# Kernel tuning notes

Hardware: AMD Instinct MI355X
Metric: run time of the kernel (lower is better)

## Reference

```python
import jax, jax.numpy as jnp
import numpy as np

TAU = 2.0  # self.temperature
EPS_GUMBEL = 1e-10
EPS_PPL = 1e-7


def setup_inputs() -> dict:
    key = jax.random.key(0)
    k1, k2, k3, k4, k5 = jax.random.split(key, 5)
    B, H = 65536, 512          # batch, conv_dim[-1]
    G, V, E = 2, 320, 256      # groups, codevectors per group, codevector_dim
    hidden_states = jax.random.normal(k1, (B, 1, H), dtype=jnp.float32)
    uniform_noise = jax.random.uniform(k2, (B, G, V), dtype=jnp.float32)
    embeddings = jax.random.uniform(k3, (G, V, E), dtype=jnp.float32, minval=-1.0, maxval=1.0)
    W_proj = jax.random.normal(k4, (G * V, H), dtype=jnp.float32) / np.sqrt(H)
    b_proj = jax.random.normal(k5, (G * V,), dtype=jnp.float32) * 0.01
    return {"hidden_states": hidden_states, "uniform_noise": uniform_noise,
            "embeddings": embeddings, "W_proj": W_proj, "b_proj": b_proj}


def reference(hidden_states, uniform_noise, embeddings, W_proj, b_proj):
    B = hidden_states.shape[0]
    G, V, E = embeddings.shape
    # weight_proj: (B, 1, H) -> (B, G*V) -> (B, G, V)
    x = hidden_states[:, 0, :]
    logits = (x @ W_proj.T + b_proj).reshape(B, G, V)
    # gumbel_softmax(tau=2, hard=True): straight-through hard one-hot
    g = -jnp.log(-jnp.log(uniform_noise + EPS_GUMBEL) + EPS_GUMBEL)
    y_soft = jax.nn.softmax((logits + g) / TAU, axis=-1)
    idx = jnp.argmax(y_soft, axis=-1)                              # (B, G)
    y_hard = jax.nn.one_hot(idx, V, dtype=y_soft.dtype)            # (B, G, V)
    gumbel_dist = y_hard - jax.lax.stop_gradient(y_soft) + y_soft  # ST estimator
    # perplexity over batch-marginal probabilities
    marginal = gumbel_dist.mean(axis=0)                            # (G, V)
    perplexity = jnp.exp(-jnp.sum(marginal * jnp.log(marginal + EPS_PPL), axis=-1)).sum()
    # select codevectors: (B, G, V) x (G, V, E) -> (B, G, E)
    selected = jnp.einsum('bgv,gve->bge', gumbel_dist, embeddings)
    return selected, perplexity
```

## Files before the change

### kernel.cpp

```cpp
#include <hip/hip_runtime.h>
#include <math.h>

#define H 512
#define GV 640
#define E_DIM 256
#define BM 64
#define KSTEP 32
#define NKT (H / KSTEP)

typedef _Float16 half8 __attribute__((ext_vector_type(8)));
typedef float f32x4 __attribute__((ext_vector_type(4)));

#define WS_WH 4096
#define WS_WL (4096 + 655360)
#define WS_NEED (4096 + 2 * 655360)

__global__ void prep_w(const float* __restrict__ W, _Float16* __restrict__ wh,
                       _Float16* __restrict__ wl)
{
    int t = blockIdx.x * 256 + threadIdx.x;
    int kt = t / 2560;
    int rem = t % 2560;
    int g = rem / 640;
    int col = rem - g * 640;
    int k = kt * KSTEP + g * 8;
    const float* src = W + (size_t)col * H + k;
    float4 v0 = *(const float4*)src;
    float4 v1 = *(const float4*)(src + 4);
    float vv[8] = {v0.x, v0.y, v0.z, v0.w, v1.x, v1.y, v1.z, v1.w};
    half8 hv, lv;
    #pragma unroll
    for (int i = 0; i < 8; ++i) {
        float ws_ = vv[i] * 1024.0f;
        _Float16 h = (_Float16)ws_;
        hv[i] = h;
        lv[i] = (_Float16)(ws_ - (float)h);
    }
    ((half8*)wh)[t] = hv;
    ((half8*)wl)[t] = lv;
}

__global__ __launch_bounds__(640) void gemm_argmax_mfma(
    const float* __restrict__ hid,
    const float* __restrict__ noise,
    const float* __restrict__ emb,
    const float* __restrict__ bias,
    const _Float16* __restrict__ wh,
    const _Float16* __restrict__ wl,
    float* __restrict__ out,
    int* __restrict__ cnt)
{
    __shared__ __align__(16) _Float16 Xh[BM][KSTEP];
    __shared__ __align__(16) _Float16 Xl[BM][KSTEP];
    __shared__ int sel_n[BM][2];

    float* red_val = (float*)&Xh[0][0];
    int*   red_idx = (int*)&Xl[0][0];

    const int tid = threadIdx.x;
    const int w = tid >> 6;
    const int l = tid & 63;
    const int q = l & 15, g = l >> 4;
    const int sig = (q >> 1) & 3;
    const int sl = (g ^ sig) * 8;
    const int brow = blockIdx.x * BM;

    f32x4 acc[4][4];
    #pragma unroll
    for (int mt = 0; mt < 4; ++mt)
        #pragma unroll
        for (int nt = 0; nt < 4; ++nt)
            acc[mt][nt] = (f32x4){0.f, 0.f, 0.f, 0.f};

    const half8* whv = (const half8*)wh;
    const half8* wlv = (const half8*)wl;

    for (int kt = 0; kt < NKT; ++kt) {
        __syncthreads();
        if (tid < 256) {
            int r = tid & 63, c = tid >> 6;
            const float* src = hid + (size_t)(brow + r) * H + kt * KSTEP + c * 8;
            float4 v0 = *(const float4*)src;
            float4 v1 = *(const float4*)(src + 4);
            float vv[8] = {v0.x, v0.y, v0.z, v0.w, v1.x, v1.y, v1.z, v1.w};
            half8 hv, lv;
            #pragma unroll
            for (int i = 0; i < 8; ++i) {
                float xs = vv[i] * 64.0f;
                _Float16 h = (_Float16)xs;
                hv[i] = h;
                lv[i] = (_Float16)(xs - (float)h);
            }
            int slot = c ^ ((r >> 1) & 3);
            *(half8*)&Xh[r][slot * 8] = hv;
            *(half8*)&Xl[r][slot * 8] = lv;
        }
        __syncthreads();

        half8 Ah[4], Al[4];
        #pragma unroll
        for (int mt = 0; mt < 4; ++mt) {
            int row = mt * 16 + q;
            Ah[mt] = *(const half8*)&Xh[row][sl];
            Al[mt] = *(const half8*)&Xl[row][sl];
        }

        const int gbase = (kt * 4 + g) * 640 + w * 64 + q;
        #pragma unroll
        for (int nt = 0; nt < 4; ++nt) {
            half8 Bh = whv[gbase + nt * 16];
            half8 Bl = wlv[gbase + nt * 16];
            #pragma unroll
            for (int mt = 0; mt < 4; ++mt) {
                acc[mt][nt] = __builtin_amdgcn_mfma_f32_16x16x32_f16(Ah[mt], Bh, acc[mt][nt], 0, 0, 0);
                acc[mt][nt] = __builtin_amdgcn_mfma_f32_16x16x32_f16(Ah[mt], Bl, acc[mt][nt], 0, 0, 0);
                acc[mt][nt] = __builtin_amdgcn_mfma_f32_16x16x32_f16(Al[mt], Bh, acc[mt][nt], 0, 0, 0);
            }
        }
    }

    __syncthreads();

    const float C1 = 1.52587890625e-05f;
    float bcol[4];
    #pragma unroll
    for (int nt = 0; nt < 4; ++nt) bcol[nt] = bias[w * 64 + nt * 16 + q];

    #pragma unroll
    for (int mt = 0; mt < 4; ++mt) {
        #pragma unroll
        for (int reg = 0; reg < 4; ++reg) {
            int r = mt * 16 + 4 * g + reg;
            float bv = -INFINITY;
            int bn = 0;
            #pragma unroll
            for (int nt = 0; nt < 4; ++nt) {
                int col = w * 64 + nt * 16 + q;
                float u = noise[(size_t)(brow + r) * GV + col];
                float gum = -logf(-logf(u + 1e-10f) + 1e-10f);
                float z = acc[mt][nt][reg] * C1 + bcol[nt] + gum;
                if (z > bv) { bv = z; bn = col; }
            }
            #pragma unroll
            for (int m = 1; m < 16; m <<= 1) {
                float ov = __shfl_xor(bv, m, 64);
                int on = __shfl_xor(bn, m, 64);
                if (ov > bv || (ov == bv && on < bn)) { bv = ov; bn = on; }
            }
            if (q == 0) { red_val[r * 10 + w] = bv; red_idx[r * 10 + w] = bn; }
        }
    }
    __syncthreads();

    if (tid < 128) {
        int r = tid >> 1, grp = tid & 1;
        float bv = -INFINITY;
        int bn = 0;
        #pragma unroll
        for (int ww = 0; ww < 5; ++ww) {
            int wi = grp * 5 + ww;
            float v = red_val[r * 10 + wi];
            int n = red_idx[r * 10 + wi];
            if (v > bv) { bv = v; bn = n; }
        }
        atomicAdd(&cnt[bn], 1);
        sel_n[r][grp] = bn;
    }
    __syncthreads();

    if (tid < 512) {
        int rg = tid >> 2, sub = tid & 3;
        int r = rg >> 1, grp = rg & 1;
        int n = sel_n[r][grp];
        const float4* src = (const float4*)(emb + (size_t)n * E_DIM);
        float4* dst = (float4*)(out + (size_t)(brow + r) * 512 + grp * 256);
        #pragma unroll
        for (int j = 0; j < 16; ++j)
            dst[sub + j * 4] = src[sub + j * 4];
    }
}

__global__ void ppl_kernel(const int* __restrict__ cnt, float* __restrict__ outp)
{
    const int lane = threadIdx.x;
    float total = 0.f;
    #pragma unroll
    for (int gg = 0; gg < 2; ++gg) {
        float s = 0.f;
        for (int v = lane; v < 320; v += 64) {
            float m = (float)cnt[gg * 320 + v] * (1.0f / 65536.0f);
            s += m * logf(m + 1e-7f);
        }
        #pragma unroll
        for (int msk = 1; msk <= 32; msk <<= 1) s += __shfl_xor(s, msk, 64);
        total += expf(-s);
    }
    if (lane == 0) *outp = total;
}

__global__ __launch_bounds__(512) void fused_gemm_argmax(
    const float* __restrict__ hid, const float* __restrict__ noise,
    const float* __restrict__ emb, const float* __restrict__ W,
    const float* __restrict__ bias, float* __restrict__ out, int* __restrict__ cnt)
{
    __shared__ float A_lds[16][64];
    __shared__ float B_lds[16][GV + 4];
    const int tid = threadIdx.x;
    const int tx = tid & 63, ty = tid >> 6;
    const int brow = blockIdx.x * 64;
    const int nbase = tx * 10;
    float acc[8][10];
    #pragma unroll
    for (int i = 0; i < 8; ++i)
        #pragma unroll
        for (int j = 0; j < 10; ++j) acc[i][j] = 0.f;
    for (int t = 0; t < H; t += 16) {
        if (t) __syncthreads();
        if (tid < 256) {
            int m = tid & 63, kq = tid >> 6;
            float4 v = *(const float4*)(hid + (size_t)(brow + m) * H + t + kq * 4);
            A_lds[kq * 4 + 0][m] = v.x; A_lds[kq * 4 + 1][m] = v.y;
            A_lds[kq * 4 + 2][m] = v.z; A_lds[kq * 4 + 3][m] = v.w;
        }
        #pragma unroll
        for (int s = 0; s < 5; ++s) {
            int c = tid + s * 512;
            int n = c % 640, kq = c / 640;
            float4 v = *(const float4*)(W + (size_t)n * H + t + kq * 4);
            B_lds[kq * 4 + 0][n] = v.x; B_lds[kq * 4 + 1][n] = v.y;
            B_lds[kq * 4 + 2][n] = v.z; B_lds[kq * 4 + 3][n] = v.w;
        }
        __syncthreads();
        #pragma unroll 4
        for (int kk = 0; kk < 16; ++kk) {
            float a[8], bb[10];
            #pragma unroll
            for (int i = 0; i < 8; ++i) a[i] = A_lds[kk][ty * 8 + i];
            #pragma unroll
            for (int j = 0; j < 10; ++j) bb[j] = B_lds[kk][nbase + j];
            #pragma unroll
            for (int i = 0; i < 8; ++i)
                #pragma unroll
                for (int j = 0; j < 10; ++j) acc[i][j] = fmaf(a[i], bb[j], acc[i][j]);
        }
    }
    float bs[10];
    #pragma unroll
    for (int j = 0; j < 10; ++j) bs[j] = bias[nbase + j];
    const int gg = tx >> 5, ll = tx & 31;
    #pragma unroll
    for (int i = 0; i < 8; ++i) {
        const int b = brow + ty * 8 + i;
        float best = -INFINITY; int bestn = nbase;
        #pragma unroll
        for (int j = 0; j < 10; ++j) {
            float u = noise[(size_t)b * GV + nbase + j];
            float gmb = -logf(-logf(u + 1e-10f) + 1e-10f);
            float z = acc[i][j] + bs[j] + gmb;
            if (z > best) { best = z; bestn = nbase + j; }
        }
        #pragma unroll
        for (int msk = 1; msk <= 16; msk <<= 1) {
            float oz = __shfl_xor(best, msk, 64);
            int on = __shfl_xor(bestn, msk, 64);
            if (oz > best || (oz == best && on < bestn)) { best = oz; bestn = on; }
        }
        if (ll == 0) atomicAdd(&cnt[bestn], 1);
        const float4* src = (const float4*)(emb + (size_t)bestn * E_DIM);
        float4* dst = (float4*)(out + (size_t)b * 512 + gg * 256);
        dst[ll] = src[ll];
        dst[ll + 32] = src[ll + 32];
    }
}

extern "C" void kernel_launch(void* const* d_in, const int* in_sizes, int n_in,
                              void* d_out, int out_size, void* d_ws, size_t ws_size,
                              hipStream_t stream)
{
    const float* hid   = (const float*)d_in[0];
    const float* noise = (const float*)d_in[1];
    const float* emb   = (const float*)d_in[2];
    const float* W     = (const float*)d_in[3];
    const float* bias  = (const float*)d_in[4];
    float* out = (float*)d_out;
    int* cnt = (int*)d_ws;
    const int B = in_sizes[0] / H;

    hipMemsetAsync(cnt, 0, GV * sizeof(int), stream);
    if (ws_size >= (size_t)WS_NEED) {
        _Float16* wh = (_Float16*)((char*)d_ws + WS_WH);
        _Float16* wl = (_Float16*)((char*)d_ws + WS_WL);
        prep_w<<<160, 256, 0, stream>>>(W, wh, wl);
        gemm_argmax_mfma<<<B / BM, 640, 0, stream>>>(hid, noise, emb, bias, wh, wl, out, cnt);
    } else {
        fused_gemm_argmax<<<B / BM, 512, 0, stream>>>(hid, noise, emb, W, bias, out, cnt);
    }
    ppl_kernel<<<1, 64, 0, stream>>>(cnt, out + (size_t)B * 512);
}
```

Baseline: 280.9 us.

## Split MFMA GEMM blocks per group and double-buffer X tile staging

Each block now handles one of the two codevector groups (320 columns, 5 waves) instead of both, doubling the grid. The hidden-state tile is double-buffered in shared memory so the next K-step's global load and fp16 split overlap the current MFMAs, which removes one barrier per iteration. In exchange, each row's hidden states are loaded and converted twice (once per group block), and the extra buffer raises LDS use.

```diff
diff --git a/kernel.cpp b/kernel.cpp
--- a/kernel.cpp
+++ b/kernel.cpp
@@ -40,7 +40,7 @@
     ((half8*)wl)[t] = lv;
 }
 
-__global__ __launch_bounds__(640) void gemm_argmax_mfma(
+__global__ __launch_bounds__(320) void gemm_argmax_mfma(
     const float* __restrict__ hid,
     const float* __restrict__ noise,
     const float* __restrict__ emb,
@@ -50,12 +50,12 @@
     float* __restrict__ out,
     int* __restrict__ cnt)
 {
-    __shared__ __align__(16) _Float16 Xh[BM][KSTEP];
-    __shared__ __align__(16) _Float16 Xl[BM][KSTEP];
-    __shared__ int sel_n[BM][2];
-
-    float* red_val = (float*)&Xh[0][0];
-    int*   red_idx = (int*)&Xl[0][0];
+    __shared__ __align__(16) _Float16 Xh[2][BM][KSTEP];
+    __shared__ __align__(16) _Float16 Xl[2][BM][KSTEP];
+    __shared__ int sel_n[BM];
+
+    float* red_val = (float*)&Xh[0][0][0];
+    int*   red_idx = (int*)&Xl[0][0][0];
 
     const int tid = threadIdx.x;
     const int w = tid >> 6;
@@ -63,7 +63,9 @@
     const int q = l & 15, g = l >> 4;
     const int sig = (q >> 1) & 3;
     const int sl = (g ^ sig) * 8;
-    const int brow = blockIdx.x * BM;
+    const int grp = blockIdx.x & 1;
+    const int brow = (blockIdx.x >> 1) * BM;
+    const int colbase = grp * 320 + w * 64 + q;
 
     f32x4 acc[4][4];
     #pragma unroll
@@ -75,13 +77,59 @@
     const half8* whv = (const half8*)wh;
     const half8* wlv = (const half8*)wl;
 
+    const int sr = tid & 63, sc = tid >> 6;
+    const int sslot = sc ^ ((sr >> 1) & 3);
+
+    if (tid < 256) {
+        const float* src = hid + (size_t)(brow + sr) * H + 0 * KSTEP + sc * 8;
+        float4 v0 = *(const float4*)src;
+        float4 v1 = *(const float4*)(src + 4);
+        float vv[8] = {v0.x, v0.y, v0.z, v0.w, v1.x, v1.y, v1.z, v1.w};
+        half8 hv, lv;
+        #pragma unroll
+        for (int i = 0; i < 8; ++i) {
+            float xs = vv[i] * 64.0f;
+            _Float16 h = (_Float16)xs;
+            hv[i] = h;
+            lv[i] = (_Float16)(xs - (float)h);
+        }
+        *(half8*)&Xh[0][sr][sslot * 8] = hv;
+        *(half8*)&Xl[0][sr][sslot * 8] = lv;
+    }
+    __syncthreads();
+
     for (int kt = 0; kt < NKT; ++kt) {
-        __syncthreads();
-        if (tid < 256) {
-            int r = tid & 63, c = tid >> 6;
-            const float* src = hid + (size_t)(brow + r) * H + kt * KSTEP + c * 8;
-            float4 v0 = *(const float4*)src;
-            float4 v1 = *(const float4*)(src + 4);
+        const int cur = kt & 1;
+        float4 v0, v1;
+        const bool do_stage = (kt + 1 < NKT) && (tid < 256);
+        if (do_stage) {
+            const float* src = hid + (size_t)(brow + sr) * H + (kt + 1) * KSTEP + sc * 8;
+            v0 = *(const float4*)src;
+            v1 = *(const float4*)(src + 4);
+        }
+
+        half8 Ah[4], Al[4];
+        #pragma unroll
+        for (int mt = 0; mt < 4; ++mt) {
+            int row = mt * 16 + q;
+            Ah[mt] = *(const half8*)&Xh[cur][row][sl];
+            Al[mt] = *(const half8*)&Xl[cur][row][sl];
+        }
+
+        const int gbase = (kt * 4 + g) * 640 + grp * 320 + w * 64 + q;
+        #pragma unroll
+        for (int nt = 0; nt < 4; ++nt) {
+            half8 Bh = whv[gbase + nt * 16];
+            half8 Bl = wlv[gbase + nt * 16];
+            #pragma unroll
+            for (int mt = 0; mt < 4; ++mt) {
+                acc[mt][nt] = __builtin_amdgcn_mfma_f32_16x16x32_f16(Ah[mt], Bh, acc[mt][nt], 0, 0, 0);
+                acc[mt][nt] = __builtin_amdgcn_mfma_f32_16x16x32_f16(Ah[mt], Bl, acc[mt][nt], 0, 0, 0);
+                acc[mt][nt] = __builtin_amdgcn_mfma_f32_16x16x32_f16(Al[mt], Bh, acc[mt][nt], 0, 0, 0);
+            }
+        }
+
+        if (do_stage) {
             float vv[8] = {v0.x, v0.y, v0.z, v0.w, v1.x, v1.y, v1.z, v1.w};
             half8 hv, lv;
             #pragma unroll
@@ -91,40 +139,16 @@
                 hv[i] = h;
                 lv[i] = (_Float16)(xs - (float)h);
             }
-            int slot = c ^ ((r >> 1) & 3);
-            *(half8*)&Xh[r][slot * 8] = hv;
-            *(half8*)&Xl[r][slot * 8] = lv;
+            *(half8*)&Xh[cur ^ 1][sr][sslot * 8] = hv;
+            *(half8*)&Xl[cur ^ 1][sr][sslot * 8] = lv;
         }
         __syncthreads();
-
-        half8 Ah[4], Al[4];
-        #pragma unroll
-        for (int mt = 0; mt < 4; ++mt) {
-            int row = mt * 16 + q;
-            Ah[mt] = *(const half8*)&Xh[row][sl];
-            Al[mt] = *(const half8*)&Xl[row][sl];
-        }
-
-        const int gbase = (kt * 4 + g) * 640 + w * 64 + q;
-        #pragma unroll
-        for (int nt = 0; nt < 4; ++nt) {
-            half8 Bh = whv[gbase + nt * 16];
-            half8 Bl = wlv[gbase + nt * 16];
-            #pragma unroll
-            for (int mt = 0; mt < 4; ++mt) {
-                acc[mt][nt] = __builtin_amdgcn_mfma_f32_16x16x32_f16(Ah[mt], Bh, acc[mt][nt], 0, 0, 0);
-                acc[mt][nt] = __builtin_amdgcn_mfma_f32_16x16x32_f16(Ah[mt], Bl, acc[mt][nt], 0, 0, 0);
-                acc[mt][nt] = __builtin_amdgcn_mfma_f32_16x16x32_f16(Al[mt], Bh, acc[mt][nt], 0, 0, 0);
-            }
-        }
-    }
-
-    __syncthreads();
+    }
 
     const float C1 = 1.52587890625e-05f;
     float bcol[4];
     #pragma unroll
-    for (int nt = 0; nt < 4; ++nt) bcol[nt] = bias[w * 64 + nt * 16 + q];
+    for (int nt = 0; nt < 4; ++nt) bcol[nt] = bias[colbase + nt * 16];
 
     #pragma unroll
     for (int mt = 0; mt < 4; ++mt) {
@@ -135,7 +159,7 @@
             int bn = 0;
             #pragma unroll
             for (int nt = 0; nt < 4; ++nt) {
-                int col = w * 64 + nt * 16 + q;
+                int col = colbase + nt * 16;
                 float u = noise[(size_t)(brow + r) * GV + col];
                 float gum = -logf(-logf(u + 1e-10f) + 1e-10f);
                 float z = acc[mt][nt][reg] * C1 + bcol[nt] + gum;
@@ -147,31 +171,29 @@
                 int on = __shfl_xor(bn, m, 64);
                 if (ov > bv || (ov == bv && on < bn)) { bv = ov; bn = on; }
             }
-            if (q == 0) { red_val[r * 10 + w] = bv; red_idx[r * 10 + w] = bn; }
+            if (q == 0) { red_val[r * 5 + w] = bv; red_idx[r * 5 + w] = bn; }
         }
     }
     __syncthreads();
 
-    if (tid < 128) {
-        int r = tid >> 1, grp = tid & 1;
+    if (tid < 64) {
+        int r = tid;
         float bv = -INFINITY;
         int bn = 0;
         #pragma unroll
         for (int ww = 0; ww < 5; ++ww) {
-            int wi = grp * 5 + ww;
-            float v = red_val[r * 10 + wi];
-            int n = red_idx[r * 10 + wi];
+            float v = red_val[r * 5 + ww];
+            int n = red_idx[r * 5 + ww];
             if (v > bv) { bv = v; bn = n; }
         }
         atomicAdd(&cnt[bn], 1);
-        sel_n[r][grp] = bn;
+        sel_n[r] = bn;
     }
     __syncthreads();
 
-    if (tid < 512) {
-        int rg = tid >> 2, sub = tid & 3;
-        int r = rg >> 1, grp = rg & 1;
-        int n = sel_n[r][grp];
+    if (tid < 256) {
+        int r = tid >> 2, sub = tid & 3;
+        int n = sel_n[r];
         const float4* src = (const float4*)(emb + (size_t)n * E_DIM);
         float4* dst = (float4*)(out + (size_t)(brow + r) * 512 + grp * 256);
         #pragma unroll
@@ -291,7 +313,7 @@
         _Float16* wh = (_Float16*)((char*)d_ws + WS_WH);
         _Float16* wl = (_Float16*)((char*)d_ws + WS_WL);
         prep_w<<<160, 256, 0, stream>>>(W, wh, wl);
-        gemm_argmax_mfma<<<B / BM, 640, 0, stream>>>(hid, noise, emb, bias, wh, wl, out, cnt);
+        gemm_argmax_mfma<<<(B / BM) * 2, 320, 0, stream>>>(hid, noise, emb, bias, wh, wl, out, cnt);
     } else {
         fused_gemm_argmax<<<B / BM, 512, 0, stream>>>(hid, noise, emb, W, bias, out, cnt);
     }
```

New measurement: 390.8 us. +39.1%, slower.

## Split GEMM-argmax blocks by codebook group to halve block size

Applied to the files above, without the earlier changes.

Each block now handles one of the two codebook groups for 64 rows, using 320 threads (5 waves) instead of 640. The grid doubles and each block only processes its group's 320 columns. The reduction and gather are simplified accordingly, and launch bounds request 4 blocks per CU. The intent is better occupancy and scheduling flexibility. The cost is that each block pair converts the same hidden-state tile to fp16, so that conversion work and those global loads are duplicated.

```diff
diff --git a/kernel.cpp b/kernel.cpp
--- a/kernel.cpp
+++ b/kernel.cpp
@@ -40,7 +40,7 @@
     ((half8*)wl)[t] = lv;
 }
 
-__global__ __launch_bounds__(640) void gemm_argmax_mfma(
+__global__ __launch_bounds__(320, 4) void gemm_argmax_mfma(
     const float* __restrict__ hid,
     const float* __restrict__ noise,
     const float* __restrict__ emb,
@@ -52,7 +52,7 @@
 {
     __shared__ __align__(16) _Float16 Xh[BM][KSTEP];
     __shared__ __align__(16) _Float16 Xl[BM][KSTEP];
-    __shared__ int sel_n[BM][2];
+    __shared__ int sel_n[BM];
 
     float* red_val = (float*)&Xh[0][0];
     int*   red_idx = (int*)&Xl[0][0];
@@ -63,7 +63,9 @@
     const int q = l & 15, g = l >> 4;
     const int sig = (q >> 1) & 3;
     const int sl = (g ^ sig) * 8;
-    const int brow = blockIdx.x * BM;
+    const int grp = blockIdx.x & 1;
+    const int brow = (blockIdx.x >> 1) * BM;
+    const int colbase = grp * 320 + w * 64 + q;
 
     f32x4 acc[4][4];
     #pragma unroll
@@ -105,7 +107,7 @@
             Al[mt] = *(const half8*)&Xl[row][sl];
         }
 
-        const int gbase = (kt * 4 + g) * 640 + w * 64 + q;
+        const int gbase = (kt * 4 + g) * 640 + grp * 320 + w * 64 + q;
         #pragma unroll
         for (int nt = 0; nt < 4; ++nt) {
             half8 Bh = whv[gbase + nt * 16];
@@ -124,7 +126,7 @@
     const float C1 = 1.52587890625e-05f;
     float bcol[4];
     #pragma unroll
-    for (int nt = 0; nt < 4; ++nt) bcol[nt] = bias[w * 64 + nt * 16 + q];
+    for (int nt = 0; nt < 4; ++nt) bcol[nt] = bias[colbase + nt * 16];
 
     #pragma unroll
     for (int mt = 0; mt < 4; ++mt) {
@@ -135,7 +137,7 @@
             int bn = 0;
             #pragma unroll
             for (int nt = 0; nt < 4; ++nt) {
-                int col = w * 64 + nt * 16 + q;
+                int col = colbase + nt * 16;
                 float u = noise[(size_t)(brow + r) * GV + col];
                 float gum = -logf(-logf(u + 1e-10f) + 1e-10f);
                 float z = acc[mt][nt][reg] * C1 + bcol[nt] + gum;
@@ -147,31 +149,29 @@
                 int on = __shfl_xor(bn, m, 64);
                 if (ov > bv || (ov == bv && on < bn)) { bv = ov; bn = on; }
             }
-            if (q == 0) { red_val[r * 10 + w] = bv; red_idx[r * 10 + w] = bn; }
+            if (q == 0) { red_val[r * 5 + w] = bv; red_idx[r * 5 + w] = bn; }
         }
     }
     __syncthreads();
 
-    if (tid < 128) {
-        int r = tid >> 1, grp = tid & 1;
+    if (tid < 64) {
+        int r = tid;
         float bv = -INFINITY;
         int bn = 0;
         #pragma unroll
         for (int ww = 0; ww < 5; ++ww) {
-            int wi = grp * 5 + ww;
-            float v = red_val[r * 10 + wi];
-            int n = red_idx[r * 10 + wi];
+            float v = red_val[r * 5 + ww];
+            int n = red_idx[r * 5 + ww];
             if (v > bv) { bv = v; bn = n; }
         }
         atomicAdd(&cnt[bn], 1);
-        sel_n[r][grp] = bn;
+        sel_n[r] = bn;
     }
     __syncthreads();
 
-    if (tid < 512) {
-        int rg = tid >> 2, sub = tid & 3;
-        int r = rg >> 1, grp = rg & 1;
-        int n = sel_n[r][grp];
+    if (tid < 256) {
+        int r = tid >> 2, sub = tid & 3;
+        int n = sel_n[r];
         const float4* src = (const float4*)(emb + (size_t)n * E_DIM);
         float4* dst = (float4*)(out + (size_t)(brow + r) * 512 + grp * 256);
         #pragma unroll
@@ -291,7 +291,7 @@
         _Float16* wh = (_Float16*)((char*)d_ws + WS_WH);
         _Float16* wl = (_Float16*)((char*)d_ws + WS_WL);
         prep_w<<<160, 256, 0, stream>>>(W, wh, wl);
-        gemm_argmax_mfma<<<B / BM, 640, 0, stream>>>(hid, noise, emb, bias, wh, wl, out, cnt);
+        gemm_argmax_mfma<<<(B / BM) * 2, 320, 0, stream>>>(hid, noise, emb, bias, wh, wl, out, cnt);
     } else {
         fused_gemm_argmax<<<B / BM, 512, 0, stream>>>(hid, noise, emb, W, bias, out, cnt);
     }
```

After: 315.3 us. +12.2%, slower.

## Split GEMM-argmax into column-blocked MFMA kernel plus separate reduce-gather kernel

Applied to the files above, without the earlier changes.

Adds a new path that tiles the 640 output columns into 10 blocks of 64, so each 256-thread workgroup computes a 64x64 tile. It loads and splits hidden states straight into registers without LDS and uses a swizzled block order. Each tile writes its partial argmax value and index to workspace, and a second kernel reduces the five partials per group, updates the counts and copies the codevector. This gives more, smaller workgroups for occupancy, at the cost of reading hidden states ten times, a round trip to workspace and an extra launch. The path runs only when the workspace is large enough.

```diff
diff --git a/kernel.cpp b/kernel.cpp
--- a/kernel.cpp
+++ b/kernel.cpp
@@ -11,9 +11,12 @@
 typedef _Float16 half8 __attribute__((ext_vector_type(8)));
 typedef float f32x4 __attribute__((ext_vector_type(4)));
 
-#define WS_WH 4096
-#define WS_WL (4096 + 655360)
-#define WS_NEED (4096 + 2 * 655360)
+#define WS_WH   4096
+#define WS_WL   (WS_WH + 655360)
+#define WS_CVAL (WS_WL + 655360)
+#define WS_CIDX (WS_CVAL + 65536 * 10 * 4)
+#define WS_NEED_FULL (WS_CIDX + 65536 * 10 * 4)
+#define WS_NEED_MID  (4096 + 2 * 655360)
 
 __global__ void prep_w(const float* __restrict__ W, _Float16* __restrict__ wh,
                        _Float16* __restrict__ wl)
@@ -40,20 +43,167 @@
     ((half8*)wl)[t] = lv;
 }
 
-__global__ __launch_bounds__(640) void gemm_argmax_mfma(
+__global__ __launch_bounds__(256) void gemm32(
     const float* __restrict__ hid,
     const float* __restrict__ noise,
-    const float* __restrict__ emb,
     const float* __restrict__ bias,
     const _Float16* __restrict__ wh,
     const _Float16* __restrict__ wl,
-    float* __restrict__ out,
-    int* __restrict__ cnt)
+    float* __restrict__ cval,
+    int* __restrict__ cidx)
+{
+    __shared__ float vlds[BM][2];
+    __shared__ int   ilds[BM][2];
+
+    const int lb = (blockIdx.x & 7) * 1280 + (blockIdx.x >> 3);
+    const int rowslice = lb / 10;
+    const int colblk = lb - rowslice * 10;
+    const int brow = rowslice * BM;
+    const int colbase = colblk * 64;
+
+    const int tid = threadIdx.x;
+    const int wid = tid >> 6;
+    const int wr = wid >> 1, wc = wid & 1;
+    const int l = tid & 63;
+    const int q = l & 15, g = l >> 4;
+
+    f32x4 acc[2][2];
+    #pragma unroll
+    for (int mt = 0; mt < 2; ++mt)
+        #pragma unroll
+        for (int nt = 0; nt < 2; ++nt)
+            acc[mt][nt] = (f32x4){0.f, 0.f, 0.f, 0.f};
+
+    const half8* whv = (const half8*)wh;
+    const half8* wlv = (const half8*)wl;
+
+    for (int kt = 0; kt < NKT; ++kt) {
+        half8 Ah[2], Al[2];
+        #pragma unroll
+        for (int mt = 0; mt < 2; ++mt) {
+            const float* aptr = hid + (size_t)(brow + wr * 32 + mt * 16 + q) * H
+                                + kt * KSTEP + g * 8;
+            float4 a0 = *(const float4*)aptr;
+            float4 a1 = *(const float4*)(aptr + 4);
+            float vv[8] = {a0.x, a0.y, a0.z, a0.w, a1.x, a1.y, a1.z, a1.w};
+            half8 hv, lv;
+            #pragma unroll
+            for (int i = 0; i < 8; ++i) {
+                float xs = vv[i] * 64.0f;
+                _Float16 h = (_Float16)xs;
+                hv[i] = h;
+                lv[i] = (_Float16)(xs - (float)h);
+            }
+            Ah[mt] = hv;
+            Al[mt] = lv;
+        }
+
+        const int gbase = (kt * 4 + g) * 640 + colbase + wc * 32 + q;
+        #pragma unroll
+        for (int nt = 0; nt < 2; ++nt) {
+            half8 Bh = whv[gbase + nt * 16];
+            half8 Bl = wlv[gbase + nt * 16];
+            #pragma unroll
+            for (int mt = 0; mt < 2; ++mt) {
+                acc[mt][nt] = __builtin_amdgcn_mfma_f32_16x16x32_f16(Ah[mt], Bh, acc[mt][nt], 0, 0, 0);
+                acc[mt][nt] = __builtin_amdgcn_mfma_f32_16x16x32_f16(Ah[mt], Bl, acc[mt][nt], 0, 0, 0);
+                acc[mt][nt] = __builtin_amdgcn_mfma_f32_16x16x32_f16(Al[mt], Bh, acc[mt][nt], 0, 0, 0);
+            }
+        }
+    }
+
+    const float C1 = 1.52587890625e-05f;
+    float bcol[2];
+    #pragma unroll
+    for (int nt = 0; nt < 2; ++nt) bcol[nt] = bias[colbase + wc * 32 + nt * 16 + q];
+
+    #pragma unroll
+    for (int mt = 0; mt < 2; ++mt) {
+        #pragma unroll
+        for (int reg = 0; reg < 4; ++reg) {
+            const int rloc = wr * 32 + mt * 16 + g * 4 + reg;
+            float bv = -INFINITY;
+            int bn = 0;
+            #pragma unroll
+            for (int nt = 0; nt < 2; ++nt) {
+                int col = colbase + wc * 32 + nt * 16 + q;
+                float u = noise[(size_t)(brow + rloc) * GV + col];
+                float gum = -logf(-logf(u + 1e-10f) + 1e-10f);
+                float z = acc[mt][nt][reg] * C1 + bcol[nt] + gum;
+                if (z > bv) { bv = z; bn = col; }
+            }
+            #pragma unroll
+            for (int m = 1; m < 16; m <<= 1) {
+                float ov = __shfl_xor(bv, m, 64);
+                int on = __shfl_xor(bn, m, 64);
+                if (ov > bv || (ov == bv && on < bn)) { bv = ov; bn = on; }
+            }
+            if (q == 0) { vlds[rloc][wc] = bv; ilds[rloc][wc] = bn; }
+        }
+    }
+    __syncthreads();
+
+    if (tid < BM) {
+        float bv = vlds[tid][0];
+        int bn = ilds[tid][0];
+        float v1 = vlds[tid][1];
+        int n1 = ilds[tid][1];
+        if (v1 > bv) { bv = v1; bn = n1; }
+        cval[(size_t)(brow + tid) * 10 + colblk] = bv;
+        cidx[(size_t)(brow + tid) * 10 + colblk] = bn;
+    }
+}
+
+__global__ __launch_bounds__(256) void reduce_gather(
+    const float* __restrict__ cval, const int* __restrict__ cidx,
+    const float* __restrict__ emb, float* __restrict__ out, int* __restrict__ cnt)
+{
+    const int tid = threadIdx.x;
+    const int task = blockIdx.x * 4 + (tid >> 6);
+    const int lane = tid & 63;
+    const int row = task >> 1, grp = task & 1;
+
+    float bv = -INFINITY;
+    int bn = 0;
+    #pragma unroll
+    for (int cb = 0; cb < 5; ++cb) {
+        float v = cval[(size_t)row * 10 + grp * 5 + cb];
+        int n = cidx[(size_t)row * 10 + grp * 5 + cb];
+        if (v > bv) { bv = v; bn = n; }
+    }
+    if (lane == 0) atomicAdd(&cnt[bn], 1);
+    const float4* src = (const float4*)(emb + (size_t)bn * E_DIM);
+    float4* dst = (float4*)(out + (size_t)row * 512 + grp * 256);
+    dst[lane] = src[lane];
+}
+
+__global__ void ppl_kernel(const int* __restrict__ cnt, float* __restrict__ outp)
+{
+    const int lane = threadIdx.x;
+    float total = 0.f;
+    #pragma unroll
+    for (int gg = 0; gg < 2; ++gg) {
+        float s = 0.f;
+        for (int v = lane; v < 320; v += 64) {
+            float m = (float)cnt[gg * 320 + v] * (1.0f / 65536.0f);
+            s += m * logf(m + 1e-7f);
+        }
+        #pragma unroll
+        for (int msk = 1; msk <= 32; msk <<= 1) s += __shfl_xor(s, msk, 64);
+        total += expf(-s);
+    }
+    if (lane == 0) *outp = total;
+}
+
+__global__ __launch_bounds__(640) void gemm_argmax_mid(
+    const float* __restrict__ hid, const float* __restrict__ noise,
+    const float* __restrict__ emb, const float* __restrict__ bias,
+    const _Float16* __restrict__ wh, const _Float16* __restrict__ wl,
+    float* __restrict__ out, int* __restrict__ cnt)
 {
     __shared__ __align__(16) _Float16 Xh[BM][KSTEP];
     __shared__ __align__(16) _Float16 Xl[BM][KSTEP];
     __shared__ int sel_n[BM][2];
-
     float* red_val = (float*)&Xh[0][0];
     int*   red_idx = (int*)&Xl[0][0];
 
@@ -69,8 +219,7 @@
     #pragma unroll
     for (int mt = 0; mt < 4; ++mt)
         #pragma unroll
-        for (int nt = 0; nt < 4; ++nt)
-            acc[mt][nt] = (f32x4){0.f, 0.f, 0.f, 0.f};
+        for (int nt = 0; nt < 4; ++nt) acc[mt][nt] = (f32x4){0.f, 0.f, 0.f, 0.f};
 
     const half8* whv = (const half8*)wh;
     const half8* wlv = (const half8*)wl;
@@ -96,7 +245,6 @@
             *(half8*)&Xl[r][slot * 8] = lv;
         }
         __syncthreads();
-
         half8 Ah[4], Al[4];
         #pragma unroll
         for (int mt = 0; mt < 4; ++mt) {
@@ -104,7 +252,6 @@
             Ah[mt] = *(const half8*)&Xh[row][sl];
             Al[mt] = *(const half8*)&Xl[row][sl];
         }
-
         const int gbase = (kt * 4 + g) * 640 + w * 64 + q;
         #pragma unroll
         for (int nt = 0; nt < 4; ++nt) {
@@ -118,14 +265,12 @@
             }
         }
     }
-
     __syncthreads();
 
     const float C1 = 1.52587890625e-05f;
     float bcol[4];
     #pragma unroll
     for (int nt = 0; nt < 4; ++nt) bcol[nt] = bias[w * 64 + nt * 16 + q];
-
     #pragma unroll
     for (int mt = 0; mt < 4; ++mt) {
         #pragma unroll
@@ -151,7 +296,6 @@
         }
     }
     __syncthreads();
-
     if (tid < 128) {
         int r = tid >> 1, grp = tid & 1;
         float bv = -INFINITY;
@@ -167,7 +311,6 @@
         sel_n[r][grp] = bn;
     }
     __syncthreads();
-
     if (tid < 512) {
         int rg = tid >> 2, sub = tid & 3;
         int r = rg >> 1, grp = rg & 1;
@@ -175,27 +318,8 @@
         const float4* src = (const float4*)(emb + (size_t)n * E_DIM);
         float4* dst = (float4*)(out + (size_t)(brow + r) * 512 + grp * 256);
         #pragma unroll
-        for (int j = 0; j < 16; ++j)
-            dst[sub + j * 4] = src[sub + j * 4];
-    }
-}
-
-__global__ void ppl_kernel(const int* __restrict__ cnt, float* __restrict__ outp)
-{
-    const int lane = threadIdx.x;
-    float total = 0.f;
-    #pragma unroll
-    for (int gg = 0; gg < 2; ++gg) {
-        float s = 0.f;
-        for (int v = lane; v < 320; v += 64) {
-            float m = (float)cnt[gg * 320 + v] * (1.0f / 65536.0f);
-            s += m * logf(m + 1e-7f);
-        }
-        #pragma unroll
-        for (int msk = 1; msk <= 32; msk <<= 1) s += __shfl_xor(s, msk, 64);
-        total += expf(-s);
-    }
-    if (lane == 0) *outp = total;
+        for (int j = 0; j < 16; ++j) dst[sub + j * 4] = src[sub + j * 4];
+    }
 }
 
 __global__ __launch_bounds__(512) void fused_gemm_argmax(
@@ -287,11 +411,19 @@
     const int B = in_sizes[0] / H;
 
     hipMemsetAsync(cnt, 0, GV * sizeof(int), stream);
-    if (ws_size >= (size_t)WS_NEED) {
+    if (ws_size >= (size_t)WS_NEED_FULL) {
+        _Float16* wh = (_Float16*)((char*)d_ws + WS_WH);
+        _Float16* wl = (_Float16*)((char*)d_ws + WS_WL);
+        float* cv = (float*)((char*)d_ws + WS_CVAL);
+        int* ci = (int*)((char*)d_ws + WS_CIDX);
+        prep_w<<<160, 256, 0, stream>>>(W, wh, wl);
+        gemm32<<<(B / BM) * 10, 256, 0, stream>>>(hid, noise, bias, wh, wl, cv, ci);
+        reduce_gather<<<(B * 2) / 4, 256, 0, stream>>>(cv, ci, emb, out, cnt);
+    } else if (ws_size >= (size_t)WS_NEED_MID) {
         _Float16* wh = (_Float16*)((char*)d_ws + WS_WH);
         _Float16* wl = (_Float16*)((char*)d_ws + WS_WL);
         prep_w<<<160, 256, 0, stream>>>(W, wh, wl);
-        gemm_argmax_mfma<<<B / BM, 640, 0, stream>>>(hid, noise, emb, bias, wh, wl, out, cnt);
+        gemm_argmax_mid<<<B / BM, 640, 0, stream>>>(hid, noise, emb, bias, wh, wl, out, cnt);
     } else {
         fused_gemm_argmax<<<B / BM, 512, 0, stream>>>(hid, noise, emb, W, bias, out, cnt);
     }
```

Result: slower. 484.0 us (+72.3%).
